# Kernel optimization log

Measured on AMD Instinct MI355X. Metric: run time of the kernel, lower is better.

## Reference

```python
import jax, jax.numpy as jnp
import numpy as np

OUT = 4096       # out_features
IN = 4096        # in_features
GS = 128         # group_size
G = IN // GS     # num_groups = 32 (IN divisible by GS -> no padding path)


def setup_inputs() -> dict:
    key = jax.random.key(0)
    k1, k2, k3 = jax.random.split(key, 3)
    x = jax.random.normal(k1, (4096, IN), dtype=jnp.float32)
    # packed int4 weights: each byte holds two 4-bit codes in [0,15] (offset-8)
    qweight = jax.random.randint(k2, (OUT, IN // 2), 0, 256, dtype=jnp.int32)
    # per-(row, group) positive scales
    scale = jax.random.uniform(k3, (OUT, G, 1), dtype=jnp.float32,
                               minval=0.01, maxval=0.1)
    return {"x": x, "qweight": qweight, "scale": scale}


def reference(x, qweight, scale):
    # unpack_int4: high nibble is the even-position element, low nibble odd
    high = (qweight >> 4) & 15
    low = qweight & 15
    q = jnp.stack([high, low], axis=-1).reshape(OUT, -1)  # [OUT, IN]
    q = q.astype(jnp.float32) - 8.0                       # back to [-8, 7]
    # group-wise dequantization
    w = q.reshape(OUT, G, GS) * scale                     # [OUT, G, GS]
    B = x.shape[0]
    xg = x.reshape(B, G, GS)                              # [B, G, GS]
    return jnp.einsum('bgs,ogs->bo', xg, w)               # [B, OUT]
```

## Files before the change

kernel.cpp:

```cpp
#include <hip/hip_runtime.h>

typedef __attribute__((ext_vector_type(8))) _Float16 f16x8;
typedef __attribute__((ext_vector_type(4))) float    f32x4;
typedef __attribute__((ext_vector_type(4))) int      i32x4;

#define IN_F   4096
#define OUT_F  4096
#define NGRP   32
#define NKT    64

#define GLOAD16(gsrc, ldst)                                                   \
    __builtin_amdgcn_global_load_lds(                                         \
        (const __attribute__((address_space(1))) unsigned int*)(gsrc),        \
        (__attribute__((address_space(3))) unsigned int*)(ldst), 16, 0, 0)

#define CFENCE  asm volatile("" ::: "memory")
#define BARRIER do { CFENCE; __builtin_amdgcn_s_barrier(); CFENCE; } while (0)
#define VMW4    asm volatile("s_waitcnt vmcnt(4)" ::: "memory")
#define SCHED0  __builtin_amdgcn_sched_barrier(0)

__global__ __launch_bounds__(256)
void prep(const float* __restrict__ X, const int* __restrict__ QW,
          const float* __restrict__ S, _Float16* __restrict__ XF,
          _Float16* __restrict__ WF) {
    if (blockIdx.x < 8192) {
        size_t i = ((size_t)blockIdx.x * 256 + threadIdx.x) * 8;
        f32x4 a = *(const f32x4*)(X + i);
        f32x4 b = *(const f32x4*)(X + i + 4);
        f16x8 h;
        h[0] = (_Float16)a[0]; h[1] = (_Float16)a[1];
        h[2] = (_Float16)a[2]; h[3] = (_Float16)a[3];
        h[4] = (_Float16)b[0]; h[5] = (_Float16)b[1];
        h[6] = (_Float16)b[2]; h[7] = (_Float16)b[3];
        *(f16x8*)(XF + i) = h;
    } else {
        size_t t  = ((size_t)blockIdx.x - 8192) * 256 + threadIdx.x;
        size_t jj = t * 4;
        size_t o  = jj >> 11;
        size_t jr = jj & 2047;
        const float s = S[o * NGRP + (jr >> 6)];
        i32x4 q = *(const i32x4*)(QW + jj);
        f16x8 h;
#pragma unroll
        for (int j = 0; j < 4; ++j) {
            const int v = q[j];
            h[2 * j]     = (_Float16)((float)(((v >> 4) & 15) - 8) * s);
            h[2 * j + 1] = (_Float16)((float)((v & 15) - 8) * s);
        }
        *(f16x8*)(WF + jj * 2) = h;
    }
}

__global__ __launch_bounds__(512, 2)
void gemm8p(const _Float16* __restrict__ A,
            const _Float16* __restrict__ B,
            float*          __restrict__ C)
{
    extern __shared__ char LDSc[];
    char* const ldsA = LDSc;
    char* const ldsB = LDSc + 65536;

    const int tid  = threadIdx.x;
    const int lane = tid & 63;
    const int wid  = tid >> 6;
    const int wm   = wid >> 2;
    const int wn   = wid & 3;

    const int bid = blockIdx.x;
    const int swz = (bid & 7) * 32 + (bid >> 3);
    const int bm0 = (swz >> 4) * 256;
    const int bn0 = (swz & 15) * 256;

    const int r0 = tid >> 3;
    const int cs = ((tid & 7) * 16) ^ ((r0 & 7) << 4);
    const _Float16* Asrc = A + (size_t)(bm0 + r0) * IN_F + (cs >> 1);
    const _Float16* Bsrc = B + (size_t)(bn0 + r0) * IN_F + (cs >> 1);
    const int dstoff = wid * 1024;

    const int lane15 = lane & 15;
    const int swr = (lane & 7) << 4;
    const int c0 = ((lane >> 4) * 16) ^ swr;
    const int c1 = (64 + (lane >> 4) * 16) ^ swr;
    int rAoff[4], rBoff[2];
#pragma unroll
    for (int mm = 0; mm < 4; ++mm) rAoff[mm] = (wm * 64 + mm * 16 + lane15) * 128;
#pragma unroll
    for (int nn = 0; nn < 2; ++nn) rBoff[nn] = (wn * 32 + nn * 16 + lane15) * 128;

    f16x8 afr[4][2], afr2[4][2], blo[2][2], bhi[2][2];
    f32x4 acc[8][4];
#pragma unroll
    for (int m = 0; m < 8; ++m)
#pragma unroll
        for (int n = 0; n < 4; ++n) acc[m][n] = (f32x4)0.0f;

#define STAGE_A(HALF, KT, BUF) do {                                           \
        const _Float16* s_ = Asrc + (size_t)(HALF) * 128 * IN_F + (KT) * 64;  \
        char* d_ = ldsA + ((BUF) * 2 + (HALF)) * 16384 + dstoff;              \
        GLOAD16(s_, d_);                                                      \
        GLOAD16(s_ + (size_t)64 * IN_F, d_ + 8192); } while (0)

#define STAGE_B(HALF, KT, BUF) do {                                           \
        const _Float16* s_ = Bsrc + (size_t)(HALF) * 128 * IN_F + (KT) * 64;  \
        char* d_ = ldsB + ((BUF) * 2 + (HALF)) * 16384 + dstoff;              \
        GLOAD16(s_, d_);                                                      \
        GLOAD16(s_ + (size_t)64 * IN_F, d_ + 8192); } while (0)

#define RD_A(BUF, QM, DST) do { char* ab_ = ldsA + ((BUF) * 2 + (QM)) * 16384;\
        _Pragma("unroll") for (int mm = 0; mm < 4; ++mm) {                    \
            DST[mm][0] = *(const f16x8*)(ab_ + rAoff[mm] + c0);               \
            DST[mm][1] = *(const f16x8*)(ab_ + rAoff[mm] + c1); } } while (0)

#define RD_B(BUF, QN, DST) do { char* bb_ = ldsB + ((BUF) * 2 + (QN)) * 16384;\
        _Pragma("unroll") for (int nn = 0; nn < 2; ++nn) {                    \
            DST[nn][0] = *(const f16x8*)(bb_ + rBoff[nn] + c0);               \
            DST[nn][1] = *(const f16x8*)(bb_ + rBoff[nn] + c1); } } while (0)

#define MFMA_Q(QM, QN, AQ, BQ)                                                \
        __builtin_amdgcn_s_setprio(1);                                        \
        _Pragma("unroll") for (int mm = 0; mm < 4; ++mm)                      \
        _Pragma("unroll") for (int nn = 0; nn < 2; ++nn)                      \
        _Pragma("unroll") for (int kk = 0; kk < 2; ++kk)                      \
            acc[(QM)*4+mm][(QN)*2+nn] =                                       \
                __builtin_amdgcn_mfma_f32_16x16x32_f16(                       \
                    AQ[mm][kk], BQ[nn][kk], acc[(QM)*4+mm][(QN)*2+nn],0,0,0); \
        __builtin_amdgcn_s_setprio(0);

    STAGE_A(0, 0, 0); STAGE_B(0, 0, 0); STAGE_B(1, 0, 0); STAGE_A(1, 0, 0);
    STAGE_A(0, 1, 1); STAGE_B(0, 1, 1); STAGE_B(1, 1, 1);
    asm volatile("s_waitcnt vmcnt(6)" ::: "memory"); BARRIER;
    RD_A(0, 0, afr); RD_B(0, 0, blo);

    for (int t = 0; t < NKT; t += 2) {
        const int k2 = (t + 2) & 63;
        const int k3 = (t + 3) & 63;
        RD_B(0, 1, bhi); STAGE_A(1, t + 1, 1);
        SCHED0; MFMA_Q(0, 0, afr, blo); BARRIER;
        RD_A(0, 1, afr2); STAGE_A(0, k2, 0);
        SCHED0; MFMA_Q(0, 1, afr, bhi); BARRIER;
        STAGE_B(0, k2, 0);
        SCHED0; MFMA_Q(1, 0, afr2, blo); VMW4; BARRIER;
        RD_A(1, 0, afr); RD_B(1, 0, blo); STAGE_B(1, k2, 0);
        SCHED0; MFMA_Q(1, 1, afr2, bhi); BARRIER;
        RD_B(1, 1, bhi); STAGE_A(1, k2, 0);
        SCHED0; MFMA_Q(0, 0, afr, blo); BARRIER;
        RD_A(1, 1, afr2); STAGE_A(0, k3, 1);
        SCHED0; MFMA_Q(0, 1, afr, bhi); BARRIER;
        STAGE_B(0, k3, 1);
        SCHED0; MFMA_Q(1, 0, afr2, blo); VMW4; BARRIER;
        RD_A(0, 0, afr); RD_B(0, 0, blo); STAGE_B(1, k3, 1);
        SCHED0; MFMA_Q(1, 1, afr2, bhi); BARRIER;
    }
    asm volatile("s_waitcnt vmcnt(0)" ::: "memory");

#pragma unroll
    for (int m = 0; m < 8; ++m) {
        const int Mr = bm0 + (m >> 2) * 128 + wm * 64 + (m & 3) * 16 + (lane >> 4) * 4;
#pragma unroll
        for (int n = 0; n < 4; ++n) {
            const int Nc = bn0 + (n >> 1) * 128 + wn * 32 + (n & 1) * 16 + lane15;
#pragma unroll
            for (int r = 0; r < 4; ++r)
                C[(size_t)(Mr + r) * OUT_F + Nc] = acc[m][n][r];
        }
    }
#undef STAGE_A
#undef STAGE_B
#undef RD_A
#undef RD_B
#undef MFMA_Q
}

__global__ __launch_bounds__(256, 3)
void gemm_f16(const _Float16* __restrict__ A,
              const _Float16* __restrict__ B,
              float*          __restrict__ C)
{
    __shared__ __align__(16) _Float16 lA[128 * 32];
    __shared__ __align__(16) _Float16 lB[128 * 32];

    const int tid  = threadIdx.x;
    const int lane = tid & 63;
    const int bid = blockIdx.x;
    const int swz = (bid & 7) * 128 + (bid >> 3);
    const int bm0 = (swz >> 5) * 128;
    const int bn0 = (swz & 31) * 128;

    const int sr = tid >> 2;
    const int sc = (tid & 3) * 8;
    const _Float16* Aps = A + (size_t)(bm0 + sr) * IN_F + sc;
    const _Float16* Bps = B + (size_t)(bn0 + sr) * IN_F + sc;
    char* lAb = (char*)lA + (tid & ~63) * 16;
    char* lBb = (char*)lB + (tid & ~63) * 16;

    const int wv = tid >> 6;
    const int wr = (wv >> 1) * 64;
    const int wc = (wv & 1)  * 64;
    const int lr  = lane & 15;
    const int lkb = (lane >> 4) * 16;

    f32x4 acc[4][4];
#pragma unroll
    for (int m = 0; m < 4; ++m)
#pragma unroll
        for (int n = 0; n < 4; ++n) acc[m][n] = (f32x4)0.0f;

    for (int kt = 0; kt < 128; ++kt) {
        __syncthreads();
        {
            const _Float16* ak = Aps + kt * 32;
            const _Float16* bk = Bps + kt * 32;
            GLOAD16(ak, lAb);
            GLOAD16(ak + (size_t)64 * IN_F, lAb + 4096);
            GLOAD16(bk, lBb);
            GLOAD16(bk + (size_t)64 * IN_F, lBb + 4096);
        }
        __syncthreads();

        f16x8 a[4], b[4];
#pragma unroll
        for (int m = 0; m < 4; ++m)
            a[m] = *(const f16x8*)((const char*)lA + (wr + m * 16 + lr) * 64 + lkb);
#pragma unroll
        for (int n = 0; n < 4; ++n)
            b[n] = *(const f16x8*)((const char*)lB + (wc + n * 16 + lr) * 64 + lkb);
#pragma unroll
        for (int m = 0; m < 4; ++m)
#pragma unroll
            for (int n = 0; n < 4; ++n)
                acc[m][n] = __builtin_amdgcn_mfma_f32_16x16x32_f16(
                    a[m], b[n], acc[m][n], 0, 0, 0);
    }

    const int crow = bm0 + wr + (lane >> 4) * 4;
    const int ccol = bn0 + wc + lr;
#pragma unroll
    for (int m = 0; m < 4; ++m)
#pragma unroll
        for (int n = 0; n < 4; ++n)
#pragma unroll
            for (int r = 0; r < 4; ++r)
                C[(size_t)(crow + m * 16 + r) * OUT_F + (ccol + n * 16)]
                    = acc[m][n][r];
}

extern "C" void kernel_launch(void* const* d_in, const int* in_sizes, int n_in,
                              void* d_out, int out_size, void* d_ws, size_t ws_size,
                              hipStream_t stream) {
    (void)in_sizes; (void)n_in; (void)out_size; (void)ws_size;
    const float* x  = (const float*)d_in[0];
    const int*   qw = (const int*)d_in[1];
    const float* s  = (const float*)d_in[2];
    float*       out = (float*)d_out;

    _Float16* xf = (_Float16*)d_ws;
    _Float16* wf = xf + (size_t)OUT_F * IN_F;
    prep<<<dim3(16384), dim3(256), 0, stream>>>(x, qw, s, xf, wf);

    hipError_t e = hipFuncSetAttribute((const void*)gemm8p,
        hipFuncAttributeMaxDynamicSharedMemorySize, 131072);
    if (e == hipSuccess)
        gemm8p<<<dim3(256), dim3(512), 131072, stream>>>(xf, wf, out);
    else
        gemm_f16<<<dim3(1024), dim3(256), 0, stream>>>(xf, wf, out);
}
```

Baseline: 147.2 us.

## Reschedule GEMM main loop staging and drop sched barriers

Reorders the global-to-LDS staging in the 8-phase GEMM loop. The prologue now prefetches the full second k-tile, and the A-half stage moves into later phases. Wait points become vmcnt(6) three times per iteration, instead of vmcnt(4) twice, to match the new outstanding-load count. The sched_barrier(0) calls before each MFMA block are removed so the compiler can interleave LDS reads and MFMAs. The aim is better overlap of memory and compute, at the risk of the compiler producing a worse schedule and of a race if the wait counts do not match the issued loads.

```diff
diff --git a/kernel.cpp b/kernel.cpp
--- a/kernel.cpp
+++ b/kernel.cpp
@@ -16,8 +16,8 @@
 
 #define CFENCE  asm volatile("" ::: "memory")
 #define BARRIER do { CFENCE; __builtin_amdgcn_s_barrier(); CFENCE; } while (0)
-#define VMW4    asm volatile("s_waitcnt vmcnt(4)" ::: "memory")
-#define SCHED0  __builtin_amdgcn_sched_barrier(0)
+#define VMW6    asm volatile("s_waitcnt vmcnt(6)" ::: "memory")
+#define VMW8    asm volatile("s_waitcnt vmcnt(8)" ::: "memory")
 
 __global__ __launch_bounds__(256)
 void prep(const float* __restrict__ X, const int* __restrict__ QW,
@@ -52,9 +52,9 @@
 }
 
 __global__ __launch_bounds__(512, 2)
-void gemm8p(const _Float16* __restrict__ A,
-            const _Float16* __restrict__ B,
-            float*          __restrict__ C)
+void gemm_ra(const _Float16* __restrict__ A,
+             const _Float16* __restrict__ B,
+             float*          __restrict__ C)
 {
     extern __shared__ char LDSc[];
     char* const ldsA = LDSc;
@@ -87,7 +87,7 @@
 #pragma unroll
     for (int nn = 0; nn < 2; ++nn) rBoff[nn] = (wn * 32 + nn * 16 + lane15) * 128;
 
-    f16x8 afr[4][2], afr2[4][2], blo[2][2], bhi[2][2];
+    f16x8 aA[4][2], aB[4][2], bA[2][2], bB[2][2];
     f32x4 acc[8][4];
 #pragma unroll
     for (int m = 0; m < 8; ++m)
@@ -127,29 +127,29 @@
         __builtin_amdgcn_s_setprio(0);
 
     STAGE_A(0, 0, 0); STAGE_B(0, 0, 0); STAGE_B(1, 0, 0); STAGE_A(1, 0, 0);
-    STAGE_A(0, 1, 1); STAGE_B(0, 1, 1); STAGE_B(1, 1, 1);
-    asm volatile("s_waitcnt vmcnt(6)" ::: "memory"); BARRIER;
-    RD_A(0, 0, afr); RD_B(0, 0, blo);
+    STAGE_A(0, 1, 1); STAGE_B(0, 1, 1); STAGE_B(1, 1, 1); STAGE_A(1, 1, 1);
+    VMW8; BARRIER;
+    RD_A(0, 0, aA); RD_B(0, 0, bA);
 
     for (int t = 0; t < NKT; t += 2) {
         const int k2 = (t + 2) & 63;
         const int k3 = (t + 3) & 63;
-        RD_B(0, 1, bhi); STAGE_A(1, t + 1, 1);
-        SCHED0; MFMA_Q(0, 0, afr, blo); BARRIER;
-        RD_A(0, 1, afr2); STAGE_A(0, k2, 0);
-        SCHED0; MFMA_Q(0, 1, afr, bhi); BARRIER;
+        RD_B(0, 1, bB);
+        MFMA_Q(0, 0, aA, bA); BARRIER;
+        RD_A(0, 1, aB); STAGE_A(0, k2, 0);
+        MFMA_Q(0, 1, aA, bB); BARRIER;
         STAGE_B(0, k2, 0);
-        SCHED0; MFMA_Q(1, 0, afr2, blo); VMW4; BARRIER;
-        RD_A(1, 0, afr); RD_B(1, 0, blo); STAGE_B(1, k2, 0);
-        SCHED0; MFMA_Q(1, 1, afr2, bhi); BARRIER;
-        RD_B(1, 1, bhi); STAGE_A(1, k2, 0);
-        SCHED0; MFMA_Q(0, 0, afr, blo); BARRIER;
-        RD_A(1, 1, afr2); STAGE_A(0, k3, 1);
-        SCHED0; MFMA_Q(0, 1, afr, bhi); BARRIER;
-        STAGE_B(0, k3, 1);
-        SCHED0; MFMA_Q(1, 0, afr2, blo); VMW4; BARRIER;
-        RD_A(0, 0, afr); RD_B(0, 0, blo); STAGE_B(1, k3, 1);
-        SCHED0; MFMA_Q(1, 1, afr2, bhi); BARRIER;
+        MFMA_Q(1, 0, aB, bA); VMW6; BARRIER;
+        RD_A(1, 0, aA); RD_B(1, 0, bA); STAGE_B(1, k2, 0); STAGE_A(1, k2, 0);
+        MFMA_Q(1, 1, aB, bB); BARRIER;
+        RD_B(1, 1, bB);
+        MFMA_Q(0, 0, aA, bA); VMW6; BARRIER;
+        RD_A(1, 1, aB); STAGE_A(0, k3, 1); STAGE_B(0, k3, 1);
+        MFMA_Q(0, 1, aA, bB); BARRIER;
+        STAGE_B(1, k3, 1);
+        MFMA_Q(1, 0, aB, bA); VMW6; BARRIER;
+        RD_A(0, 0, aA); RD_B(0, 0, bA); STAGE_A(1, k3, 1);
+        MFMA_Q(1, 1, aB, bB); BARRIER;
     }
     asm volatile("s_waitcnt vmcnt(0)" ::: "memory");
 
@@ -257,10 +257,10 @@
     _Float16* wf = xf + (size_t)OUT_F * IN_F;
     prep<<<dim3(16384), dim3(256), 0, stream>>>(x, qw, s, xf, wf);
 
-    hipError_t e = hipFuncSetAttribute((const void*)gemm8p,
+    hipError_t e = hipFuncSetAttribute((const void*)gemm_ra,
         hipFuncAttributeMaxDynamicSharedMemorySize, 131072);
     if (e == hipSuccess)
-        gemm8p<<<dim3(256), dim3(512), 131072, stream>>>(xf, wf, out);
+        gemm_ra<<<dim3(256), dim3(512), 131072, stream>>>(xf, wf, out);
     else
         gemm_f16<<<dim3(1024), dim3(256), 0, stream>>>(xf, wf, out);
 }
```

After: 138.9 us. -5.6%, faster.
